# Kernel optimization log

Hardware: AMD Instinct MI355X
Metric: run time of the kernel (lower is better)

## Reference

```python
import jax, jax.numpy as jnp
import numpy as np


def setup_inputs() -> dict:
    key = jax.random.key(0)
    k1, k2 = jax.random.split(key)
    B, N, F = 16, 4096, 512
    S, K = 8, 1024          # splits, symbols per codebook
    D = F // S              # sub-vector dim
    x = jax.random.normal(k1, (B, N, F), dtype=jnp.float32)
    # torch init: uniform(-1/symbols, 1/symbols)
    codebooks = jax.random.uniform(k2, (S, K, D), dtype=jnp.float32,
                                   minval=-1.0 / K, maxval=1.0 / K)
    return {"x": x, "codebooks": codebooks}


def reference(x, codebooks):
    B, N, F = x.shape
    S, K, D = codebooks.shape
    xs = x.reshape(B, N, S, D)                       # split into S chunks
    x2 = jnp.sum(xs * xs, axis=-1, keepdims=True)    # [B,N,S,1]
    c2 = jnp.sum(codebooks * codebooks, axis=-1)     # [S,K]
    xc = jnp.einsum('bnsd,skd->bnsk', xs, codebooks)
    dist = x2 + c2[None, None] - 2.0 * xc            # [B,N,S,K]
    idx = jnp.argmin(dist, axis=-1)                  # [B,N,S]
    # gather chosen code vectors per split -> [B,N,S,D]
    sym = codebooks[jnp.arange(S)[None, None, :], idx]
    sg = jax.lax.stop_gradient
    # straight-through quantized output
    quant = (xs + sg(sym - xs)).reshape(B, N, F)
    # per-split mse (mean over B,N,D of each chunk), summed over splits
    dev = (jnp.sum(jnp.mean((sym - sg(xs)) ** 2, axis=(0, 1, 3)))
           + 0.25 * jnp.sum(jnp.mean((xs - sg(sym)) ** 2, axis=(0, 1, 3))))
    return quant, dev
```

## Files before the change

kernel.cpp:

```cpp
#include <hip/hip_runtime.h>
#include <cstdint>

constexpr int Bv = 16, Nv = 4096, Fv = 512, Sv = 8, Kv = 1024, Dv = 64;
constexpr int Mv = Bv * Nv;
#define BDIM 512
constexpr int RG = 4;

using bf16x8 = __attribute__((ext_vector_type(8))) short;
using f32x4  = __attribute__((ext_vector_type(4))) float;
typedef unsigned short u16;
typedef unsigned int u32;

__device__ __forceinline__ u16 bf16rne(float f) {
  union { float f; u32 u; } v; v.f = f;
  u32 u = v.u + 0x7FFFu + ((v.u >> 16) & 1u);
  return (u16)(u >> 16);
}

__device__ __forceinline__ void gload_lds16(const void* g, void* lds) {
  __builtin_amdgcn_global_load_lds(
      (const __attribute__((address_space(1))) void*)g,
      (__attribute__((address_space(3))) void*)lds, 16, 0, 0);
}
__device__ __forceinline__ void gload_lds4(const void* g, void* lds) {
  __builtin_amdgcn_global_load_lds(
      (const __attribute__((address_space(1))) void*)g,
      (__attribute__((address_space(3))) void*)lds, 4, 0, 0);
}

__global__ void prep_kernel(const float* __restrict__ cb, u16* __restrict__ swz,
                            float* __restrict__ c2m) {
  int idx = blockIdx.x * 256 + threadIdx.x;
  int cw = idx & (Kv - 1);
  const float4* src = (const float4*)(cb + (size_t)idx * Dv);
  float v[64];
  float s2 = 0.f;
#pragma unroll
  for (int i = 0; i < 16; ++i) {
    float4 f = src[i];
    v[i * 4 + 0] = f.x; v[i * 4 + 1] = f.y; v[i * 4 + 2] = f.z; v[i * 4 + 3] = f.w;
    s2 += f.x * f.x + f.y * f.y + f.z * f.z + f.w * f.w;
  }
  c2m[idx] = -0.5f * s2;
  uint4* out = (uint4*)(swz + (size_t)idx * Dv);
#pragma unroll
  for (int slot = 0; slot < 8; ++slot) {
    int slotp = slot ^ (cw & 7);
    u32 w[4];
#pragma unroll
    for (int p = 0; p < 4; ++p)
      w[p] = (u32)bf16rne(v[slot * 8 + p * 2]) | ((u32)bf16rne(v[slot * 8 + p * 2 + 1]) << 16);
    uint4 pk; pk.x = w[0]; pk.y = w[1]; pk.z = w[2]; pk.w = w[3];
    out[slotp] = pk;
  }
}

__global__ __launch_bounds__(BDIM, 2) void pq_mfma(
    const float* __restrict__ x, const float* __restrict__ cb,
    const u16* __restrict__ swz, const float* __restrict__ c2m_g,
    float* __restrict__ quant, float* __restrict__ devpart) {
  __shared__ __attribute__((aligned(16))) u16 cw_lds[Kv * Dv];
  __shared__ __attribute__((aligned(16))) float c2_lds[Kv];

  const int tid = threadIdx.x;
  const int s = blockIdx.x & 7;
  const int chunk = blockIdx.x >> 3;
  const int wave = tid >> 6, lane = tid & 63;
  const int l15 = lane & 15, lg = lane >> 4;
  const int slotp0 = lg ^ (l15 & 7);
  const int slotp1 = (4 + lg) ^ (l15 & 7);

  const u16* swz_s = swz + (size_t)s * Kv * Dv;
#pragma unroll
  for (int it = 0; it < 16; ++it)
    gload_lds16(swz_s + (size_t)(it * BDIM + tid) * 8,
                &cw_lds[(it * BDIM + (tid & ~63)) * 8]);
#pragma unroll
  for (int it = 0; it < 2; ++it)
    gload_lds4(c2m_g + s * Kv + it * BDIM + tid,
               &c2_lds[it * BDIM + (tid & ~63)]);

  float4 xr[2 * RG];
  const float* xbase0 = x + (size_t)(chunk * 1024 + wave * 64) * Fv + s * Dv;
#pragma unroll
  for (int rg = 0; rg < RG; ++rg) {
    const float* xp = xbase0 + (size_t)(rg * 16 + l15) * Fv + lg * 8;
    xr[rg * 2] = *(const float4*)xp;
    xr[rg * 2 + 1] = *(const float4*)(xp + 4);
  }

  __syncthreads();

  const u16* r0 = cw_lds + l15 * Dv + slotp0 * 8;
  const u16* r1 = cw_lds + l15 * Dv + slotp1 * 8;

  float devacc = 0.f;

#pragma unroll 1
  for (int u = 0; u < 2; ++u) {
    const int rowu = chunk * 1024 + u * 512 + wave * 64;

    bf16x8 xf[RG][2];
    float x2p[RG];
#pragma unroll
    for (int rg = 0; rg < RG; ++rg) {
      float4 f0 = xr[rg * 2], f1 = xr[rg * 2 + 1];
      x2p[rg] = f0.x * f0.x + f0.y * f0.y + f0.z * f0.z + f0.w * f0.w
              + f1.x * f1.x + f1.y * f1.y + f1.z * f1.z + f1.w * f1.w;
      bf16x8 v;
      v[0] = (short)bf16rne(f0.x); v[1] = (short)bf16rne(f0.y);
      v[2] = (short)bf16rne(f0.z); v[3] = (short)bf16rne(f0.w);
      v[4] = (short)bf16rne(f1.x); v[5] = (short)bf16rne(f1.y);
      v[6] = (short)bf16rne(f1.z); v[7] = (short)bf16rne(f1.w);
      xf[rg][0] = v;
      const float* xp = x + (size_t)(rowu + rg * 16 + l15) * Fv + s * Dv + 32 + lg * 8;
      float4 g0 = *(const float4*)xp;
      float4 g1 = *(const float4*)(xp + 4);
      x2p[rg] += g0.x * g0.x + g0.y * g0.y + g0.z * g0.z + g0.w * g0.w
               + g1.x * g1.x + g1.y * g1.y + g1.z * g1.z + g1.w * g1.w;
      bf16x8 w;
      w[0] = (short)bf16rne(g0.x); w[1] = (short)bf16rne(g0.y);
      w[2] = (short)bf16rne(g0.z); w[3] = (short)bf16rne(g0.w);
      w[4] = (short)bf16rne(g1.x); w[5] = (short)bf16rne(g1.y);
      w[6] = (short)bf16rne(g1.z); w[7] = (short)bf16rne(g1.w);
      xf[rg][1] = w;
    }

    float bv[RG];
#pragma unroll
    for (int rg = 0; rg < RG; ++rg) bv[rg] = -3.0e38f;

    bf16x8 aE0, aE1, aO0, aO1;
    f32x4 c2E, c2O;
    aE0 = *(const bf16x8*)r0;
    aE1 = *(const bf16x8*)r1;
    c2E = *(const f32x4*)&c2_lds[lg * 4];

    auto readO = [&](int t1) {
      aO0 = *(const bf16x8*)(r0 + t1 * 16 * Dv);
      aO1 = *(const bf16x8*)(r1 + t1 * 16 * Dv);
      c2O = *(const f32x4*)&c2_lds[t1 * 16 + lg * 4];
    };
    auto readE = [&](int t1) {
      aE0 = *(const bf16x8*)(r0 + t1 * 16 * Dv);
      aE1 = *(const bf16x8*)(r1 + t1 * 16 * Dv);
      c2E = *(const f32x4*)&c2_lds[t1 * 16 + lg * 4];
    };
    auto computeE = [&](int t) {
      const u32 kb = (u32)(t * 16) | (u32)(lg * 4);
      __builtin_amdgcn_s_setprio(1);
#pragma unroll
      for (int rg = 0; rg < RG; ++rg) {
        f32x4 acc = __builtin_amdgcn_mfma_f32_16x16x32_bf16(aE0, xf[rg][0], c2E, 0, 0, 0);
        acc = __builtin_amdgcn_mfma_f32_16x16x32_bf16(aE1, xf[rg][1], acc, 0, 0, 0);
        float p0 = __builtin_bit_cast(float, __builtin_bit_cast(u32, acc[0]) | kb);
        float p1 = __builtin_bit_cast(float, __builtin_bit_cast(u32, acc[1]) | (kb | 1u));
        float p2 = __builtin_bit_cast(float, __builtin_bit_cast(u32, acc[2]) | (kb | 2u));
        float p3 = __builtin_bit_cast(float, __builtin_bit_cast(u32, acc[3]) | (kb | 3u));
        bv[rg] = fmaxf(fmaxf(fmaxf(p0, p1), fmaxf(p2, p3)), bv[rg]);
      }
      __builtin_amdgcn_s_setprio(0);
    };
    auto computeO = [&](int t) {
      const u32 kb = (u32)(t * 16) | (u32)(lg * 4);
      __builtin_amdgcn_s_setprio(1);
#pragma unroll
      for (int rg = 0; rg < RG; ++rg) {
        f32x4 acc = __builtin_amdgcn_mfma_f32_16x16x32_bf16(aO0, xf[rg][0], c2O, 0, 0, 0);
        acc = __builtin_amdgcn_mfma_f32_16x16x32_bf16(aO1, xf[rg][1], acc, 0, 0, 0);
        float p0 = __builtin_bit_cast(float, __builtin_bit_cast(u32, acc[0]) | kb);
        float p1 = __builtin_bit_cast(float, __builtin_bit_cast(u32, acc[1]) | (kb | 1u));
        float p2 = __builtin_bit_cast(float, __builtin_bit_cast(u32, acc[2]) | (kb | 2u));
        float p3 = __builtin_bit_cast(float, __builtin_bit_cast(u32, acc[3]) | (kb | 3u));
        bv[rg] = fmaxf(fmaxf(fmaxf(p0, p1), fmaxf(p2, p3)), bv[rg]);
      }
      __builtin_amdgcn_s_setprio(0);
    };

#pragma unroll 1
    for (int t = 0; t < 62; t += 2) {
      readO(t + 1);
      computeE(t);
      readE(t + 2);
      computeO(t + 1);
    }
    readO(63);
    computeE(62);
    computeO(63);

#pragma unroll
    for (int rg = 0; rg < RG; ++rg) {
      float b = bv[rg], xx = x2p[rg];
      b = fmaxf(b, __shfl_xor(b, 16, 64)); xx += __shfl_xor(xx, 16, 64);
      b = fmaxf(b, __shfl_xor(b, 32, 64)); xx += __shfl_xor(xx, 32, 64);
      bv[rg] = b; x2p[rg] = xx;
    }
#pragma unroll
    for (int rg = 0; rg < RG; ++rg) devacc += x2p[rg] - 2.f * bv[rg];

    if (u == 0) {
      const float* xb = x + (size_t)(chunk * 1024 + 512 + wave * 64) * Fv + s * Dv;
#pragma unroll
      for (int rg = 0; rg < RG; ++rg) {
        const float* xp = xb + (size_t)(rg * 16 + l15) * Fv + lg * 8;
        xr[rg * 2] = *(const float4*)xp;
        xr[rg * 2 + 1] = *(const float4*)(xp + 4);
      }
    }

    const float* cbs = cb + (size_t)s * Kv * Dv;
    float* qbase = quant + (size_t)rowu * Fv + s * Dv;
#pragma unroll
    for (int i = 0; i < 16; ++i) {
      int rl = i * 4 + lg;
      int kk = __shfl(__builtin_bit_cast(int, bv[i >> 2]), 4 * (i & 3) + lg, 64) & 1023;
      f32x4 v = *(const f32x4*)(cbs + (size_t)kk * Dv + l15 * 4);
      __builtin_nontemporal_store(v, (f32x4*)(qbase + (size_t)rl * Fv + l15 * 4));
    }
  }

#pragma unroll
  for (int m = 1; m <= 8; m <<= 1) devacc += __shfl_xor(devacc, m, 64);
  if (lane == 0) devpart[(size_t)blockIdx.x * 8 + wave] = devacc;
}

__global__ void dev_reduce(const float* __restrict__ part, float* __restrict__ out) {
  __shared__ float sred[256];
  int tid = threadIdx.x;
  float s = 0.f;
  for (int i = tid; i < 4096; i += 256) s += part[i];
  sred[tid] = s;
  __syncthreads();
  for (int off = 128; off > 0; off >>= 1) {
    if (tid < off) sred[tid] += sred[tid + off];
    __syncthreads();
  }
  if (tid == 0) out[0] = sred[0] * (1.25f / 4194304.0f);
}

extern "C" void kernel_launch(void* const* d_in, const int* in_sizes, int n_in,
                              void* d_out, int out_size, void* d_ws, size_t ws_size,
                              hipStream_t stream) {
  const float* x = (const float*)d_in[0];
  const float* cb = (const float*)d_in[1];
  float* quant = (float*)d_out;
  float* dev = quant + (size_t)Mv * Fv;

  u16* swz = (u16*)d_ws;
  float* c2m = (float*)(swz + (size_t)Sv * Kv * Dv);
  float* part = c2m + Sv * Kv;

  prep_kernel<<<(Sv * Kv) / 256, 256, 0, stream>>>(cb, swz, c2m);
  pq_mfma<<<512, BDIM, 0, stream>>>(x, cb, swz, c2m, quant, part);
  dev_reduce<<<1, 256, 0, stream>>>(part, dev);
}
```

Baseline: 107.2 us.

## Software-pipeline MFMA and argmin epilogue, prefetch full x rows, use packed bf16 convert

```diff
diff --git a/kernel.cpp b/kernel.cpp
--- a/kernel.cpp
+++ b/kernel.cpp
@@ -15,6 +15,12 @@
   union { float f; u32 u; } v; v.f = f;
   u32 u = v.u + 0x7FFFu + ((v.u >> 16) & 1u);
   return (u16)(u >> 16);
+}
+
+__device__ __forceinline__ u32 cvtpk(float lo, float hi) {
+  u32 r;
+  asm("v_cvt_pk_bf16_f32 %0, %1, %2" : "=v"(r) : "v"(lo), "v"(hi));
+  return r;
 }
 
 __device__ __forceinline__ void gload_lds16(const void* g, void* lds) {
@@ -80,13 +86,17 @@
     gload_lds4(c2m_g + s * Kv + it * BDIM + tid,
                &c2_lds[it * BDIM + (tid & ~63)]);
 
-  float4 xr[2 * RG];
-  const float* xbase0 = x + (size_t)(chunk * 1024 + wave * 64) * Fv + s * Dv;
-#pragma unroll
-  for (int rg = 0; rg < RG; ++rg) {
-    const float* xp = xbase0 + (size_t)(rg * 16 + l15) * Fv + lg * 8;
-    xr[rg * 2] = *(const float4*)xp;
-    xr[rg * 2 + 1] = *(const float4*)(xp + 4);
+  float4 xr[RG][4];
+  {
+    const float* xb = x + (size_t)(chunk * 1024 + wave * 64) * Fv + s * Dv;
+#pragma unroll
+    for (int rg = 0; rg < RG; ++rg) {
+      const float* xp = xb + (size_t)(rg * 16 + l15) * Fv + lg * 8;
+      xr[rg][0] = *(const float4*)xp;
+      xr[rg][1] = *(const float4*)(xp + 4);
+      xr[rg][2] = *(const float4*)(xp + 32);
+      xr[rg][3] = *(const float4*)(xp + 36);
+    }
   }
 
   __syncthreads();
@@ -94,36 +104,28 @@
   const u16* r0 = cw_lds + l15 * Dv + slotp0 * 8;
   const u16* r1 = cw_lds + l15 * Dv + slotp1 * 8;
 
-  float devacc = 0.f;
+  const u32 lgr0 = (u32)(lg * 4), lgr1 = lgr0 | 1u, lgr2 = lgr0 | 2u, lgr3 = lgr0 | 3u;
+  float devx2 = 0.f, bvsum = 0.f;
 
 #pragma unroll 1
   for (int u = 0; u < 2; ++u) {
     const int rowu = chunk * 1024 + u * 512 + wave * 64;
 
     bf16x8 xf[RG][2];
-    float x2p[RG];
 #pragma unroll
     for (int rg = 0; rg < RG; ++rg) {
-      float4 f0 = xr[rg * 2], f1 = xr[rg * 2 + 1];
-      x2p[rg] = f0.x * f0.x + f0.y * f0.y + f0.z * f0.z + f0.w * f0.w
-              + f1.x * f1.x + f1.y * f1.y + f1.z * f1.z + f1.w * f1.w;
-      bf16x8 v;
-      v[0] = (short)bf16rne(f0.x); v[1] = (short)bf16rne(f0.y);
-      v[2] = (short)bf16rne(f0.z); v[3] = (short)bf16rne(f0.w);
-      v[4] = (short)bf16rne(f1.x); v[5] = (short)bf16rne(f1.y);
-      v[6] = (short)bf16rne(f1.z); v[7] = (short)bf16rne(f1.w);
-      xf[rg][0] = v;
-      const float* xp = x + (size_t)(rowu + rg * 16 + l15) * Fv + s * Dv + 32 + lg * 8;
-      float4 g0 = *(const float4*)xp;
-      float4 g1 = *(const float4*)(xp + 4);
-      x2p[rg] += g0.x * g0.x + g0.y * g0.y + g0.z * g0.z + g0.w * g0.w
-               + g1.x * g1.x + g1.y * g1.y + g1.z * g1.z + g1.w * g1.w;
-      bf16x8 w;
-      w[0] = (short)bf16rne(g0.x); w[1] = (short)bf16rne(g0.y);
-      w[2] = (short)bf16rne(g0.z); w[3] = (short)bf16rne(g0.w);
-      w[4] = (short)bf16rne(g1.x); w[5] = (short)bf16rne(g1.y);
-      w[6] = (short)bf16rne(g1.z); w[7] = (short)bf16rne(g1.w);
-      xf[rg][1] = w;
+#pragma unroll
+      for (int h = 0; h < 2; ++h) {
+        float4 f0 = xr[rg][h * 2], f1 = xr[rg][h * 2 + 1];
+        devx2 += f0.x * f0.x + f0.y * f0.y + f0.z * f0.z + f0.w * f0.w
+               + f1.x * f1.x + f1.y * f1.y + f1.z * f1.z + f1.w * f1.w;
+        union { u32 w[4]; bf16x8 v; } cvt;
+        cvt.w[0] = cvtpk(f0.x, f0.y);
+        cvt.w[1] = cvtpk(f0.z, f0.w);
+        cvt.w[2] = cvtpk(f1.x, f1.y);
+        cvt.w[3] = cvtpk(f1.z, f1.w);
+        xf[rg][h] = cvt.v;
+      }
     }
 
     float bv[RG];
@@ -132,79 +134,97 @@
 
     bf16x8 aE0, aE1, aO0, aO1;
     f32x4 c2E, c2O;
-    aE0 = *(const bf16x8*)r0;
-    aE1 = *(const bf16x8*)r1;
-    c2E = *(const f32x4*)&c2_lds[lg * 4];
-
-    auto readO = [&](int t1) {
-      aO0 = *(const bf16x8*)(r0 + t1 * 16 * Dv);
-      aO1 = *(const bf16x8*)(r1 + t1 * 16 * Dv);
-      c2O = *(const f32x4*)&c2_lds[t1 * 16 + lg * 4];
-    };
-    auto readE = [&](int t1) {
-      aE0 = *(const bf16x8*)(r0 + t1 * 16 * Dv);
-      aE1 = *(const bf16x8*)(r1 + t1 * 16 * Dv);
-      c2E = *(const f32x4*)&c2_lds[t1 * 16 + lg * 4];
-    };
-    auto computeE = [&](int t) {
-      const u32 kb = (u32)(t * 16) | (u32)(lg * 4);
+    f32x4 accE[RG], accO[RG];
+
+    auto readE = [&](int t) {
+      aE0 = *(const bf16x8*)(r0 + t * 16 * Dv);
+      aE1 = *(const bf16x8*)(r1 + t * 16 * Dv);
+      c2E = *(const f32x4*)&c2_lds[t * 16 + lg * 4];
+    };
+    auto readO = [&](int t) {
+      aO0 = *(const bf16x8*)(r0 + t * 16 * Dv);
+      aO1 = *(const bf16x8*)(r1 + t * 16 * Dv);
+      c2O = *(const f32x4*)&c2_lds[t * 16 + lg * 4];
+    };
+    auto mfmaE = [&]() {
       __builtin_amdgcn_s_setprio(1);
 #pragma unroll
+      for (int rg = 0; rg < RG; ++rg)
+        accE[rg] = __builtin_amdgcn_mfma_f32_16x16x32_bf16(aE0, xf[rg][0], c2E, 0, 0, 0);
+#pragma unroll
+      for (int rg = 0; rg < RG; ++rg)
+        accE[rg] = __builtin_amdgcn_mfma_f32_16x16x32_bf16(aE1, xf[rg][1], accE[rg], 0, 0, 0);
+      __builtin_amdgcn_s_setprio(0);
+    };
+    auto mfmaO = [&]() {
+      __builtin_amdgcn_s_setprio(1);
+#pragma unroll
+      for (int rg = 0; rg < RG; ++rg)
+        accO[rg] = __builtin_amdgcn_mfma_f32_16x16x32_bf16(aO0, xf[rg][0], c2O, 0, 0, 0);
+#pragma unroll
+      for (int rg = 0; rg < RG; ++rg)
+        accO[rg] = __builtin_amdgcn_mfma_f32_16x16x32_bf16(aO1, xf[rg][1], accO[rg], 0, 0, 0);
+      __builtin_amdgcn_s_setprio(0);
+    };
+    auto procE = [&](int tp) {
+      const u32 tb = (u32)(tp << 4);
+#pragma unroll
       for (int rg = 0; rg < RG; ++rg) {
-        f32x4 acc = __builtin_amdgcn_mfma_f32_16x16x32_bf16(aE0, xf[rg][0], c2E, 0, 0, 0);
-        acc = __builtin_amdgcn_mfma_f32_16x16x32_bf16(aE1, xf[rg][1], acc, 0, 0, 0);
-        float p0 = __builtin_bit_cast(float, __builtin_bit_cast(u32, acc[0]) | kb);
-        float p1 = __builtin_bit_cast(float, __builtin_bit_cast(u32, acc[1]) | (kb | 1u));
-        float p2 = __builtin_bit_cast(float, __builtin_bit_cast(u32, acc[2]) | (kb | 2u));
-        float p3 = __builtin_bit_cast(float, __builtin_bit_cast(u32, acc[3]) | (kb | 3u));
-        bv[rg] = fmaxf(fmaxf(fmaxf(p0, p1), fmaxf(p2, p3)), bv[rg]);
-      }
-      __builtin_amdgcn_s_setprio(0);
-    };
-    auto computeO = [&](int t) {
-      const u32 kb = (u32)(t * 16) | (u32)(lg * 4);
-      __builtin_amdgcn_s_setprio(1);
+        float p0 = __builtin_bit_cast(float, (__builtin_bit_cast(u32, accE[rg][0]) | tb) | lgr0);
+        float p1 = __builtin_bit_cast(float, (__builtin_bit_cast(u32, accE[rg][1]) | tb) | lgr1);
+        float p2 = __builtin_bit_cast(float, (__builtin_bit_cast(u32, accE[rg][2]) | tb) | lgr2);
+        float p3 = __builtin_bit_cast(float, (__builtin_bit_cast(u32, accE[rg][3]) | tb) | lgr3);
+        float m = fmaxf(fmaxf(p0, p1), p2);
+        bv[rg] = fmaxf(fmaxf(m, p3), bv[rg]);
+      }
+    };
+    auto procO = [&](int tp) {
+      const u32 tb = (u32)(tp << 4);
 #pragma unroll
       for (int rg = 0; rg < RG; ++rg) {
-        f32x4 acc = __builtin_amdgcn_mfma_f32_16x16x32_bf16(aO0, xf[rg][0], c2O, 0, 0, 0);
-        acc = __builtin_amdgcn_mfma_f32_16x16x32_bf16(aO1, xf[rg][1], acc, 0, 0, 0);
-        float p0 = __builtin_bit_cast(float, __builtin_bit_cast(u32, acc[0]) | kb);
-        float p1 = __builtin_bit_cast(float, __builtin_bit_cast(u32, acc[1]) | (kb | 1u));
-        float p2 = __builtin_bit_cast(float, __builtin_bit_cast(u32, acc[2]) | (kb | 2u));
-        float p3 = __builtin_bit_cast(float, __builtin_bit_cast(u32, acc[3]) | (kb | 3u));
-        bv[rg] = fmaxf(fmaxf(fmaxf(p0, p1), fmaxf(p2, p3)), bv[rg]);
-      }
-      __builtin_amdgcn_s_setprio(0);
-    };
-
+        float p0 = __builtin_bit_cast(float, (__builtin_bit_cast(u32, accO[rg][0]) | tb) | lgr0);
+        float p1 = __builtin_bit_cast(float, (__builtin_bit_cast(u32, accO[rg][1]) | tb) | lgr1);
+        float p2 = __builtin_bit_cast(float, (__builtin_bit_cast(u32, accO[rg][2]) | tb) | lgr2);
+        float p3 = __builtin_bit_cast(float, (__builtin_bit_cast(u32, accO[rg][3]) | tb) | lgr3);
+        float m = fmaxf(fmaxf(p0, p1), p2);
+        bv[rg] = fmaxf(fmaxf(m, p3), bv[rg]);
+      }
+    };
+
+    readE(0);
+    mfmaE();
 #pragma unroll 1
-    for (int t = 0; t < 62; t += 2) {
-      readO(t + 1);
-      computeE(t);
-      readE(t + 2);
-      computeO(t + 1);
+    for (int t = 1; t < 63; t += 2) {
+      readO(t);
+      mfmaO();
+      procE(t - 1);
+      readE(t + 1);
+      mfmaE();
+      procO(t);
     }
     readO(63);
-    computeE(62);
-    computeO(63);
+    mfmaO();
+    procE(62);
+    procO(63);
 
 #pragma unroll
     for (int rg = 0; rg < RG; ++rg) {
-      float b = bv[rg], xx = x2p[rg];
-      b = fmaxf(b, __shfl_xor(b, 16, 64)); xx += __shfl_xor(xx, 16, 64);
-      b = fmaxf(b, __shfl_xor(b, 32, 64)); xx += __shfl_xor(xx, 32, 64);
-      bv[rg] = b; x2p[rg] = xx;
-    }
-#pragma unroll
-    for (int rg = 0; rg < RG; ++rg) devacc += x2p[rg] - 2.f * bv[rg];
+      float b = bv[rg];
+      b = fmaxf(b, __shfl_xor(b, 16, 64));
+      b = fmaxf(b, __shfl_xor(b, 32, 64));
+      bv[rg] = b;
+      bvsum += b;
+    }
 
     if (u == 0) {
       const float* xb = x + (size_t)(chunk * 1024 + 512 + wave * 64) * Fv + s * Dv;
 #pragma unroll
       for (int rg = 0; rg < RG; ++rg) {
         const float* xp = xb + (size_t)(rg * 16 + l15) * Fv + lg * 8;
-        xr[rg * 2] = *(const float4*)xp;
-        xr[rg * 2 + 1] = *(const float4*)(xp + 4);
+        xr[rg][0] = *(const float4*)xp;
+        xr[rg][1] = *(const float4*)(xp + 4);
+        xr[rg][2] = *(const float4*)(xp + 32);
+        xr[rg][3] = *(const float4*)(xp + 36);
       }
     }
 
@@ -220,8 +240,11 @@
   }
 
 #pragma unroll
-  for (int m = 1; m <= 8; m <<= 1) devacc += __shfl_xor(devacc, m, 64);
-  if (lane == 0) devpart[(size_t)blockIdx.x * 8 + wave] = devacc;
+  for (int m = 1; m <= 32; m <<= 1) devx2 += __shfl_xor(devx2, m, 64);
+#pragma unroll
+  for (int m = 1; m <= 8; m <<= 1) bvsum += __shfl_xor(bvsum, m, 64);
+  if (lane == 0)
+    devpart[(size_t)blockIdx.x * 8 + wave] = devx2 - 2.f * bvsum;
 }
 
 __global__ void dev_reduce(const float* __restrict__ part, float* __restrict__ out) {
```

Result: faster. 104.7 us (-2.4%).
